# Performance work log

Hardware: AMD Instinct MI355X
Metric: run time of the kernel (lower is better)

The kernel has to match this reference:

```python
import jax, jax.numpy as jnp
import numpy as np

B, T, D_IN, D_OUT = 8, 4096, 512, 512
STYLE, RANK, ALPHA = 256, 8, 1.0
NUM_LORA = (D_IN + D_OUT) * RANK


def setup_inputs() -> dict:
    key = jax.random.key(0)
    ks = jax.random.split(key, 8)
    s = 0.02
    return {
        "x": jax.random.normal(ks[0], (B, T, D_IN), jnp.float32),
        "style_emb": jax.random.normal(ks[1], (B, STYLE), jnp.float32),
        "w_base": jax.random.normal(ks[2], (D_OUT, D_IN), jnp.float32) * s,
        "b_base": jax.random.normal(ks[3], (D_OUT,), jnp.float32) * s,
        "w_h1": jax.random.normal(ks[4], (STYLE, STYLE), jnp.float32) * s,
        "b_h1": jax.random.normal(ks[5], (STYLE,), jnp.float32) * s,
        "w_h2": jax.random.normal(ks[6], (NUM_LORA, STYLE), jnp.float32) * s,
        "b_h2": jax.random.normal(ks[7], (NUM_LORA,), jnp.float32) * s,
    }


def reference(x, style_emb, w_base, b_base, w_h1, b_h1, w_h2, b_h2):
    # Base linear: [B,T,D_out]
    base_out = jnp.einsum("btd,od->bto", x, w_base) + b_base
    # Hypernet: Linear -> SiLU -> Linear producing per-sample LoRA params
    h = jax.nn.silu(style_emb @ w_h1.T + b_h1)          # [B, STYLE]
    raw = h @ w_h2.T + b_h2                             # [B, NUM_LORA]
    split = D_IN * RANK
    mat_a = raw[:, :split].reshape(B, RANK, D_IN)       # [B, r, D_in]
    mat_b = raw[:, split:].reshape(B, D_OUT, RANK)      # [B, D_out, r]
    # Low-rank path: x @ A^T @ B^T  (never materialize [B,D_out,D_in])
    down = jnp.einsum("btd,brd->btr", x, mat_a)         # [B, T, r]
    lora = jnp.einsum("btr,bor->bto", down, mat_b)      # [B, T, D_out]
    return base_out + ALPHA * lora
```

## Files before the change

### kernel.cpp

```cpp
#include <hip/hip_runtime.h>
#include <hip/hip_fp16.h>
#include <stdint.h>


#define NB 8
#define NT 4096
#define DIN 512
#define DOUT 512
#define NSTYLE 256
#define RANK 8
#define NLORA ((DIN + DOUT) * RANK)

typedef _Float16 f16x8 __attribute__((ext_vector_type(8)));
typedef float f32x4 __attribute__((ext_vector_type(4)));

__global__ void k_hyper1(const float* __restrict__ style,
                         const float* __restrict__ w_h1,
                         const float* __restrict__ b_h1,
                         float* __restrict__ h) {
  const int b = blockIdx.x;
  const int j = threadIdx.x;
  __shared__ float s[NSTYLE];
  s[j] = style[b * NSTYLE + j];
  __syncthreads();
  const float4* wrow = (const float4*)(w_h1 + (size_t)j * NSTYLE);
  float acc = b_h1[j];
#pragma unroll 8
  for (int k = 0; k < NSTYLE / 4; ++k) {
    float4 w4 = wrow[k];
    acc += s[4 * k + 0] * w4.x + s[4 * k + 1] * w4.y + s[4 * k + 2] * w4.z +
           s[4 * k + 3] * w4.w;
  }
  h[b * NSTYLE + j] = acc / (1.f + expf(-acc));
}

__global__ __launch_bounds__(256) void k_hyper2(const float* __restrict__ h,
                                                const float* __restrict__ w_h2,
                                                const float* __restrict__ b_h2,
                                                float* __restrict__ raw) {
  __shared__ float hs[NB * NSTYLE];
  const int t = threadIdx.x;
#pragma unroll
  for (int i = 0; i < NB * NSTYLE / 256; ++i) hs[i * 256 + t] = h[i * 256 + t];
  __syncthreads();
  const int w = t >> 6, lane = t & 63;
  const int n = blockIdx.x * 4 + w;
  float4 w4 = *(const float4*)(w_h2 + (size_t)n * NSTYLE + lane * 4);
  float acc[NB];
#pragma unroll
  for (int b = 0; b < NB; ++b) {
    float4 hb = *(const float4*)(&hs[b * NSTYLE + lane * 4]);
    acc[b] = hb.x * w4.x + hb.y * w4.y + hb.z * w4.z + hb.w * w4.w;
#pragma unroll
    for (int m = 32; m > 0; m >>= 1) acc[b] += __shfl_xor(acc[b], m);
  }
  if (lane == 0) {
    const float bb = b_h2[n];
#pragma unroll
    for (int b = 0; b < NB; ++b) raw[(size_t)b * NLORA + n] = acc[b] + bb;
  }
}

__global__ void k_weff(const float* __restrict__ raw,
                       const float* __restrict__ w_base,
                       _Float16* __restrict__ Whf) {
  const int cg = blockIdx.x;
  const int b = blockIdx.y;
  const int t = threadIdx.x;
  __shared__ float Als[RANK * DIN];
  __shared__ float Wbs[16 * 516];
  __shared__ float Bls[16][RANK];
  const float* rb = raw + (size_t)b * NLORA;
#pragma unroll
  for (int i = 0; i < 4; ++i)
    *(float4*)(&Als[(i * 256 + t) * 4]) = *(const float4*)(&rb[(i * 256 + t) * 4]);
#pragma unroll
  for (int i = 0; i < 8; ++i) {
    int fi = i * 256 + t;
    int oo = fi >> 7, d4 = fi & 127;
    float4 v = *(const float4*)(&w_base[((size_t)(cg * 16 + oo)) * DIN + d4 * 4]);
    *(float4*)(&Wbs[oo * 516 + d4 * 4]) = v;
  }
  if (t < 16 * RANK) {
    int oo = t >> 3, r = t & 7;
    Bls[oo][r] = rb[DIN * RANK + (cg * 16 + oo) * RANK + r];
  }
  __syncthreads();
  const int lane = t & 63;
  const int oo = lane & 15;
  const int koff = ((lane >> 4) & 3) * 8;
  float br[RANK];
#pragma unroll
  for (int r = 0; r < RANK; ++r) br[r] = Bls[oo][r];
  _Float16* dst = Whf + (size_t)b * (DOUT * DIN) + cg * 8192;
#pragma unroll
  for (int i = 0; i < 4; ++i) {
    const int q = i * 256 + t;
    const int kkg = q >> 6;
    const int kb = kkg * 32 + koff;
    f16x8 v;
#pragma unroll
    for (int j = 0; j < 8; ++j) {
      float a = Wbs[oo * 516 + kb + j];
#pragma unroll
      for (int r = 0; r < RANK; ++r) a += br[r] * Als[r * DIN + kb + j];
      v[j] = (_Float16)a;
    }
    *(f16x8*)(dst + (size_t)q * 8) = v;
  }
}

#define BM 128
#define BN 128
#define BK 64

__global__ __launch_bounds__(256) void k_gemm(
    const float* __restrict__ x, const _Float16* __restrict__ Whf,
    const float* __restrict__ b_base, float* __restrict__ out) {
  const int id = blockIdx.x;
  const int b = id & 7;
  const int nt = (id >> 3) & 3;
  const int mt = id >> 5;
  const int t = threadIdx.x;
  const int lane = t & 63;
  const int wave = t >> 6;
  const int wr = wave >> 1, wc = wave & 1;
  const int l16 = lane & 15, lq = lane >> 4;

  __shared__ _Float16 Xs[BM * BK];
  __shared__ _Float16 Ws[BN * BK];

  const float* xb = x + ((size_t)b * NT + (size_t)mt * BM) * DIN;
  const _Float16* wbt = Whf + (size_t)b * (DOUT * DIN) + (size_t)(nt * 8) * 8192;

  f32x4 acc[4][4];
#pragma unroll
  for (int m = 0; m < 4; ++m)
#pragma unroll
    for (int n = 0; n < 4; ++n)
#pragma unroll
      for (int j = 0; j < 4; ++j) acc[m][n][j] = 0.f;

  for (int step = 0; step < DIN / BK; ++step) {
    __syncthreads();
#pragma unroll
    for (int i = 0; i < 4; ++i) {
      const int p = i * 256 + t;
      const int row = p >> 3, o8 = p & 7;
      const float* src = xb + (size_t)row * DIN + step * BK + o8 * 8;
      float4 f0 = *(const float4*)(src);
      float4 f1 = *(const float4*)(src + 4);
      f16x8 hh;
      hh[0] = (_Float16)f0.x; hh[1] = (_Float16)f0.y;
      hh[2] = (_Float16)f0.z; hh[3] = (_Float16)f0.w;
      hh[4] = (_Float16)f1.x; hh[5] = (_Float16)f1.y;
      hh[6] = (_Float16)f1.z; hh[7] = (_Float16)f1.w;
      const int byte = (row * 128 + o8 * 16) ^ ((row & 7) << 4);
      *(f16x8*)((char*)Xs + byte) = hh;
    }
#pragma unroll
    for (int i = 0; i < 4; ++i) {
      const int c = i * 256 + t;
      const int cgr = c >> 7, kkr = (c >> 6) & 1, e = c & 63;
      const _Float16* g = wbt + (size_t)cgr * 8192 + (size_t)(step * 2 + kkr) * 512 + e * 8;
      __builtin_amdgcn_global_load_lds(
          (const __attribute__((address_space(1))) void*)g,
          (__attribute__((address_space(3))) void*)((char*)Ws +
                                                    (i * 256 + wave * 64) * 16),
          16, 0, 0);
    }
    __syncthreads();
#pragma unroll
    for (int kk = 0; kk < 2; ++kk) {
      f16x8 af[4], bf[4];
#pragma unroll
      for (int m = 0; m < 4; ++m) {
        const int row = wr * 64 + m * 16 + l16;
        const int byte = (row * 128 + (kk * 4 + lq) * 16) ^ ((row & 7) << 4);
        af[m] = *(const f16x8*)((const char*)Xs + byte);
      }
#pragma unroll
      for (int n = 0; n < 4; ++n)
        bf[n] = *(const f16x8*)((const char*)Ws +
                                (((wc * 4 + n) * 2 + kk) * 1024 + lane * 16));
#pragma unroll
      for (int m = 0; m < 4; ++m)
#pragma unroll
        for (int n = 0; n < 4; ++n)
          acc[m][n] = __builtin_amdgcn_mfma_f32_16x16x32_f16(af[m], bf[n],
                                                             acc[m][n], 0, 0, 0);
    }
  }

  float bv[4];
#pragma unroll
  for (int n = 0; n < 4; ++n)
    bv[n] = b_base[nt * BN + wc * 64 + n * 16 + l16];

#pragma unroll
  for (int m = 0; m < 4; ++m) {
#pragma unroll
    for (int j = 0; j < 4; ++j) {
      const int r = mt * BM + wr * 64 + m * 16 + lq * 4 + j;
      float* orow = out + ((size_t)b * NT + r) * DOUT + nt * BN;
#pragma unroll
      for (int n = 0; n < 4; ++n)
        orow[wc * 64 + n * 16 + l16] = acc[m][n][j] + bv[n];
    }
  }
}

extern "C" void kernel_launch(void* const* d_in, const int* in_sizes, int n_in,
                              void* d_out, int out_size, void* d_ws,
                              size_t ws_size, hipStream_t stream) {
  const float* x = (const float*)d_in[0];
  const float* style = (const float*)d_in[1];
  const float* w_base = (const float*)d_in[2];
  const float* b_base = (const float*)d_in[3];
  const float* w_h1 = (const float*)d_in[4];
  const float* b_h1 = (const float*)d_in[5];
  const float* w_h2 = (const float*)d_in[6];
  const float* b_h2 = (const float*)d_in[7];
  float* out = (float*)d_out;

  char* ws = (char*)d_ws;
  float* h = (float*)ws;
  float* raw = (float*)(ws + 8192);
  _Float16* Whf = (_Float16*)(ws + 8192 + 262144);

  k_hyper1<<<NB, NSTYLE, 0, stream>>>(style, w_h1, b_h1, h);
  k_hyper2<<<NLORA / 4, 256, 0, stream>>>(h, w_h2, b_h2, raw);
  k_weff<<<dim3(DOUT / 16, NB), 256, 0, stream>>>(raw, w_base, Whf);
  k_gemm<<<(NT / BM) * (DOUT / BN) * NB, 256, 0, stream>>>(x, Whf, b_base, out);
}
```

Baseline: 181.2 us.

## Double-buffer LDS tiles in GEMM to overlap global loads with MFMA

The GEMM main loop now keeps two LDS buffers for the X and W tiles. The next K-step's fp32 x is loaded into registers, and W is prefetched into the alternate buffer via global_load_lds, both before the current step's MFMAs. The converted x is written to LDS after compute, which leaves one barrier per step instead of two. This hides global memory latency behind compute, at the cost of double the LDS (64KB) and extra registers, which may reduce occupancy.

New measurement: 181.8 us. No clear change (+0.3%).

```diff
diff --git a/kernel.cpp b/kernel.cpp
--- a/kernel.cpp
+++ b/kernel.cpp
@@ -127,8 +127,8 @@
   const int wr = wave >> 1, wc = wave & 1;
   const int l16 = lane & 15, lq = lane >> 4;
 
-  __shared__ _Float16 Xs[BM * BK];
-  __shared__ _Float16 Ws[BN * BK];
+  __shared__ _Float16 Xs[2][BM * BK];
+  __shared__ _Float16 Ws[2][BN * BK];
 
   const float* xb = x + ((size_t)b * NT + (size_t)mt * BM) * DIN;
   const _Float16* wbt = Whf + (size_t)b * (DOUT * DIN) + (size_t)(nt * 8) * 8192;
@@ -141,35 +141,66 @@
 #pragma unroll
       for (int j = 0; j < 4; ++j) acc[m][n][j] = 0.f;
 
+
+  f32x4 xf[4][2];
+
+#pragma unroll
+  for (int i = 0; i < 4; ++i) {
+    const int p = i * 256 + t;
+    const float* src = xb + (size_t)(p >> 3) * DIN + (p & 7) * 8;
+    xf[i][0] = *(const f32x4*)(src);
+    xf[i][1] = *(const f32x4*)(src + 4);
+  }
+#pragma unroll
+  for (int i = 0; i < 4; ++i) {
+    const int c = i * 256 + t;
+    const _Float16* g = wbt + (size_t)(c >> 7) * 8192 +
+                        (size_t)((c >> 6) & 1) * 512 + (c & 63) * 8;
+    __builtin_amdgcn_global_load_lds(
+        (const __attribute__((address_space(1))) void*)g,
+        (__attribute__((address_space(3))) void*)((char*)Ws[0] +
+                                                  (i * 256 + wave * 64) * 16),
+        16, 0, 0);
+  }
+#pragma unroll
+  for (int i = 0; i < 4; ++i) {
+    const int p = i * 256 + t;
+    const int row = p >> 3, o8 = p & 7;
+    f16x8 hh;
+    hh[0] = (_Float16)xf[i][0][0]; hh[1] = (_Float16)xf[i][0][1];
+    hh[2] = (_Float16)xf[i][0][2]; hh[3] = (_Float16)xf[i][0][3];
+    hh[4] = (_Float16)xf[i][1][0]; hh[5] = (_Float16)xf[i][1][1];
+    hh[6] = (_Float16)xf[i][1][2]; hh[7] = (_Float16)xf[i][1][3];
+    const int byte = (row * 128 + o8 * 16) ^ ((row & 7) << 4);
+    *(f16x8*)((char*)Xs[0] + byte) = hh;
+  }
+  __syncthreads();
+
   for (int step = 0; step < DIN / BK; ++step) {
-    __syncthreads();
-#pragma unroll
-    for (int i = 0; i < 4; ++i) {
-      const int p = i * 256 + t;
-      const int row = p >> 3, o8 = p & 7;
-      const float* src = xb + (size_t)row * DIN + step * BK + o8 * 8;
-      float4 f0 = *(const float4*)(src);
-      float4 f1 = *(const float4*)(src + 4);
-      f16x8 hh;
-      hh[0] = (_Float16)f0.x; hh[1] = (_Float16)f0.y;
-      hh[2] = (_Float16)f0.z; hh[3] = (_Float16)f0.w;
-      hh[4] = (_Float16)f1.x; hh[5] = (_Float16)f1.y;
-      hh[6] = (_Float16)f1.z; hh[7] = (_Float16)f1.w;
-      const int byte = (row * 128 + o8 * 16) ^ ((row & 7) << 4);
-      *(f16x8*)((char*)Xs + byte) = hh;
-    }
-#pragma unroll
-    for (int i = 0; i < 4; ++i) {
-      const int c = i * 256 + t;
-      const int cgr = c >> 7, kkr = (c >> 6) & 1, e = c & 63;
-      const _Float16* g = wbt + (size_t)cgr * 8192 + (size_t)(step * 2 + kkr) * 512 + e * 8;
-      __builtin_amdgcn_global_load_lds(
-          (const __attribute__((address_space(1))) void*)g,
-          (__attribute__((address_space(3))) void*)((char*)Ws +
-                                                    (i * 256 + wave * 64) * 16),
-          16, 0, 0);
-    }
-    __syncthreads();
+    const int cur = step & 1;
+    const bool pf = step < DIN / BK - 1;
+    if (pf) {
+#pragma unroll
+      for (int i = 0; i < 4; ++i) {
+        const int p = i * 256 + t;
+        const float* src =
+            xb + (size_t)(p >> 3) * DIN + (step + 1) * BK + (p & 7) * 8;
+        xf[i][0] = *(const f32x4*)(src);
+        xf[i][1] = *(const f32x4*)(src + 4);
+      }
+#pragma unroll
+      for (int i = 0; i < 4; ++i) {
+        const int c = i * 256 + t;
+        const _Float16* g = wbt + (size_t)(c >> 7) * 8192 +
+                            (size_t)((step + 1) * 2 + ((c >> 6) & 1)) * 512 +
+                            (c & 63) * 8;
+        __builtin_amdgcn_global_load_lds(
+            (const __attribute__((address_space(1))) void*)g,
+            (__attribute__((address_space(3))) void*)((char*)Ws[cur ^ 1] +
+                                                      (i * 256 + wave * 64) * 16),
+            16, 0, 0);
+      }
+    }
 #pragma unroll
     for (int kk = 0; kk < 2; ++kk) {
       f16x8 af[4], bf[4];
@@ -177,11 +208,11 @@
       for (int m = 0; m < 4; ++m) {
         const int row = wr * 64 + m * 16 + l16;
         const int byte = (row * 128 + (kk * 4 + lq) * 16) ^ ((row & 7) << 4);
-        af[m] = *(const f16x8*)((const char*)Xs + byte);
+        af[m] = *(const f16x8*)((const char*)Xs[cur] + byte);
       }
 #pragma unroll
       for (int n = 0; n < 4; ++n)
-        bf[n] = *(const f16x8*)((const char*)Ws +
+        bf[n] = *(const f16x8*)((const char*)Ws[cur] +
                                 (((wc * 4 + n) * 2 + kk) * 1024 + lane * 16));
 #pragma unroll
       for (int m = 0; m < 4; ++m)
@@ -190,6 +221,21 @@
           acc[m][n] = __builtin_amdgcn_mfma_f32_16x16x32_f16(af[m], bf[n],
                                                              acc[m][n], 0, 0, 0);
     }
+    if (pf) {
+#pragma unroll
+      for (int i = 0; i < 4; ++i) {
+        const int p = i * 256 + t;
+        const int row = p >> 3, o8 = p & 7;
+        f16x8 hh;
+        hh[0] = (_Float16)xf[i][0][0]; hh[1] = (_Float16)xf[i][0][1];
+        hh[2] = (_Float16)xf[i][0][2]; hh[3] = (_Float16)xf[i][0][3];
+        hh[4] = (_Float16)xf[i][1][0]; hh[5] = (_Float16)xf[i][1][1];
+        hh[6] = (_Float16)xf[i][1][2]; hh[7] = (_Float16)xf[i][1][3];
+        const int byte = (row * 128 + o8 * 16) ^ ((row & 7) << 4);
+        *(f16x8*)((char*)Xs[cur ^ 1] + byte) = hh;
+      }
+    }
+    __syncthreads();
   }
 
   float bv[4];
```
